# Performance work log

Hardware: AMD Instinct MI355X
Metric: run time of the kernel (lower is better)

Reference implementation:

```python
import jax, jax.numpy as jnp
import numpy as np

B, C, H, W = 64, 3, 384, 384


def setup_inputs() -> dict:
    key = jax.random.key(0)
    k1, k2 = jax.random.split(key)
    imgs = jax.random.normal(k1, (B, C, H, W), dtype=jnp.float32)
    eye = jnp.broadcast_to(jnp.eye(2, 3, dtype=jnp.float32), (B, 2, 3))
    theta = eye + 0.05 * jax.random.normal(k2, (B, 2, 3), dtype=jnp.float32)
    return {"imgs": imgs, "theta": theta}


def _gen_affine_grid(theta, h, w):
    # Mirrors torchvision functional_tensor._gen_affine_grid (align_corners=False style).
    # theta: [2,3]; returns normalized grid [h, w, 2] in [-1, 1].
    d = 0.5
    xs = jnp.linspace(-w * 0.5 + d, w * 0.5 + d - 1, w, dtype=jnp.float32)  # [w]
    ys = jnp.linspace(-h * 0.5 + d, h * 0.5 + d - 1, h, dtype=jnp.float32)  # [h]
    # base_grid[y, x] = (xs[x], ys[y], 1)
    xg, yg = jnp.meshgrid(xs, ys)  # each [h, w]
    ones = jnp.ones_like(xg)
    base = jnp.stack([xg, yg, ones], axis=-1)  # [h, w, 3]
    scale = jnp.array([0.5 * w, 0.5 * h], dtype=jnp.float32)
    rescaled_theta = theta.T / scale  # [3, 2]
    return base @ rescaled_theta  # [h, w, 2]


def _grid_sample_bilinear(img, grid):
    # img: [C, H, W], grid: [H, W, 2] normalized coords, zeros padding,
    # align_corners=False (torch grid_sample semantics).
    c, h, w = img.shape
    ix = (grid[..., 0] + 1.0) * w * 0.5 - 0.5  # [H, W]
    iy = (grid[..., 1] + 1.0) * h * 0.5 - 0.5
    x0 = jnp.floor(ix)
    y0 = jnp.floor(iy)
    wx1 = ix - x0
    wy1 = iy - y0
    wx0 = 1.0 - wx1
    wy0 = 1.0 - wy1

    def gather(xi, yi):
        valid = (xi >= 0) & (xi < w) & (yi >= 0) & (yi < h)
        xc = jnp.clip(xi, 0, w - 1).astype(jnp.int32)
        yc = jnp.clip(yi, 0, h - 1).astype(jnp.int32)
        v = img[:, yc, xc]  # [C, H, W] gather
        return v * valid.astype(img.dtype)

    out = (gather(x0, y0) * (wx0 * wy0)
           + gather(x0 + 1, y0) * (wx1 * wy0)
           + gather(x0, y0 + 1) * (wx0 * wy1)
           + gather(x0 + 1, y0 + 1) * (wx1 * wy1))
    return out  # [C, H, W]


def reference(imgs, theta):
    b, c, h, w = imgs.shape

    def per_image(img, th):
        grid = _gen_affine_grid(th, h, w)
        return _grid_sample_bilinear(img, grid)

    return jax.vmap(per_image)(imgs, theta)  # [B, C, H, W]
```

## Files before the change

kernel.cpp:

```cpp
#include <hip/hip_runtime.h>

#define B_ 64
#define C_ 3
#define H_ 384
#define W_ 384
#define HW_ (H_ * W_)

__global__ __launch_bounds__(256) void affine_sample_kernel(
    const float* __restrict__ imgs,
    const float* __restrict__ theta,
    float* __restrict__ out)
{
    int nb = gridDim.x;
    int bid = blockIdx.x;
    int sb = (bid & 7) * (nb >> 3) + (bid >> 3);

    int idx = sb * 256 + threadIdx.x;
    int x = idx % W_;
    int t = idx / W_;
    int y = t % H_;
    int b = t / H_;
    b = __builtin_amdgcn_readfirstlane(b);

    const float* th = theta + b * 6;
    float t00 = th[0], t01 = th[1], t02 = th[2];
    float t10 = th[3], t11 = th[4], t12 = th[5];

    float xg = (float)x - 191.5f;
    float yg = (float)y - 191.5f;

    float ix = fmaf(xg, t00, fmaf(yg, t01, t02)) + 191.5f;
    float iy = fmaf(xg, t10, fmaf(yg, t11, t12)) + 191.5f;

    float x0f = floorf(ix);
    float y0f = floorf(iy);
    float wx1 = ix - x0f;
    float wy1 = iy - y0f;
    float wx0 = 1.0f - wx1;
    float wy0 = 1.0f - wy1;
    float x1f = x0f + 1.0f;
    float y1f = y0f + 1.0f;

    bool vx0 = (x0f >= 0.0f) && (x0f < (float)W_);
    bool vx1 = (x1f >= 0.0f) && (x1f < (float)W_);
    bool vy0 = (y0f >= 0.0f) && (y0f < (float)H_);
    bool vy1 = (y1f >= 0.0f) && (y1f < (float)H_);

    int x0 = (int)fminf(fmaxf(x0f, 0.0f), (float)(W_ - 1));
    int x1 = (int)fminf(fmaxf(x1f, 0.0f), (float)(W_ - 1));
    int y0 = (int)fminf(fmaxf(y0f, 0.0f), (float)(H_ - 1));
    int y1 = (int)fminf(fmaxf(y1f, 0.0f), (float)(H_ - 1));

    float w00 = wx0 * wy0 * ((vx0 && vy0) ? 1.0f : 0.0f);
    float w01 = wx1 * wy0 * ((vx1 && vy0) ? 1.0f : 0.0f);
    float w10 = wx0 * wy1 * ((vx0 && vy1) ? 1.0f : 0.0f);
    float w11 = wx1 * wy1 * ((vx1 && vy1) ? 1.0f : 0.0f);

    int o00 = y0 * W_ + x0;
    int o01 = y0 * W_ + x1;
    int o10 = y1 * W_ + x0;
    int o11 = y1 * W_ + x1;

    const float* bimg = imgs + (size_t)b * (C_ * HW_);
    float* bout = out + (size_t)b * (C_ * HW_) + y * W_ + x;

    float v[C_][4];
#pragma unroll
    for (int c = 0; c < C_; ++c) {
        const float* p = bimg + c * HW_;
        v[c][0] = p[o00];
        v[c][1] = p[o01];
        v[c][2] = p[o10];
        v[c][3] = p[o11];
    }

#pragma unroll
    for (int c = 0; c < C_; ++c) {
        float r = fmaf(v[c][0], w00, fmaf(v[c][1], w01,
                  fmaf(v[c][2], w10, v[c][3] * w11)));
        bout[c * HW_] = r;
    }
}

extern "C" void kernel_launch(void* const* d_in, const int* in_sizes, int n_in,
                              void* d_out, int out_size, void* d_ws, size_t ws_size,
                              hipStream_t stream) {
    const float* imgs = (const float*)d_in[0];
    const float* theta = (const float*)d_in[1];
    float* out = (float*)d_out;
    int total = B_ * H_ * W_;
    affine_sample_kernel<<<total / 256, 256, 0, stream>>>(imgs, theta, out);
}
```

Baseline: 224.1 us.

## Process 2x2 output pixels per thread with vector nontemporal stores

Each thread now computes a 2x2 block of output pixels, so a 192-thread block covers two full rows, and the grid shrinks to one block per row pair. The four bilinear setups share the theta loads and index math, and the outputs go out as 2-wide vector nontemporal stores. The aim is fewer threads, wider stores, and more independent gathers in flight per thread. In exchange, register pressure rises and each wave's gather addresses span two rows, which may change cache locality.

Measured after the change: 253.2 us. 1.13x slower.

```diff
diff --git a/kernel.cpp b/kernel.cpp
--- a/kernel.cpp
+++ b/kernel.cpp
@@ -6,29 +6,15 @@
 #define W_ 384
 #define HW_ (H_ * W_)
 
-__global__ __launch_bounds__(256) void affine_sample_kernel(
-    const float* __restrict__ imgs,
-    const float* __restrict__ theta,
-    float* __restrict__ out)
+typedef float f32x2 __attribute__((ext_vector_type(2)));
+
+struct Pix { float w00, w01, w10, w11; int o00, o01, o10, o11; };
+
+__device__ __forceinline__ Pix pix_setup(
+    float xg, float yg,
+    float t00, float t01, float t02,
+    float t10, float t11, float t12)
 {
-    int nb = gridDim.x;
-    int bid = blockIdx.x;
-    int sb = (bid & 7) * (nb >> 3) + (bid >> 3);
-
-    int idx = sb * 256 + threadIdx.x;
-    int x = idx % W_;
-    int t = idx / W_;
-    int y = t % H_;
-    int b = t / H_;
-    b = __builtin_amdgcn_readfirstlane(b);
-
-    const float* th = theta + b * 6;
-    float t00 = th[0], t01 = th[1], t02 = th[2];
-    float t10 = th[3], t11 = th[4], t12 = th[5];
-
-    float xg = (float)x - 191.5f;
-    float yg = (float)y - 191.5f;
-
     float ix = fmaf(xg, t00, fmaf(yg, t01, t02)) + 191.5f;
     float iy = fmaf(xg, t10, fmaf(yg, t11, t12)) + 191.5f;
 
@@ -51,34 +37,66 @@
     int y0 = (int)fminf(fmaxf(y0f, 0.0f), (float)(H_ - 1));
     int y1 = (int)fminf(fmaxf(y1f, 0.0f), (float)(H_ - 1));
 
-    float w00 = wx0 * wy0 * ((vx0 && vy0) ? 1.0f : 0.0f);
-    float w01 = wx1 * wy0 * ((vx1 && vy0) ? 1.0f : 0.0f);
-    float w10 = wx0 * wy1 * ((vx0 && vy1) ? 1.0f : 0.0f);
-    float w11 = wx1 * wy1 * ((vx1 && vy1) ? 1.0f : 0.0f);
+    Pix p;
+    p.w00 = wx0 * wy0 * ((vx0 && vy0) ? 1.0f : 0.0f);
+    p.w01 = wx1 * wy0 * ((vx1 && vy0) ? 1.0f : 0.0f);
+    p.w10 = wx0 * wy1 * ((vx0 && vy1) ? 1.0f : 0.0f);
+    p.w11 = wx1 * wy1 * ((vx1 && vy1) ? 1.0f : 0.0f);
+    p.o00 = y0 * W_ + x0;
+    p.o01 = y0 * W_ + x1;
+    p.o10 = y1 * W_ + x0;
+    p.o11 = y1 * W_ + x1;
+    return p;
+}
 
-    int o00 = y0 * W_ + x0;
-    int o01 = y0 * W_ + x1;
-    int o10 = y1 * W_ + x0;
-    int o11 = y1 * W_ + x1;
+__global__ __launch_bounds__(192) void affine_sample_kernel(
+    const float* __restrict__ imgs,
+    const float* __restrict__ theta,
+    float* __restrict__ out)
+{
+    int nb = gridDim.x;
+    int bid = blockIdx.x;
+    int sb = (bid & 7) * (nb >> 3) + (bid >> 3);
+
+    int b  = sb / 192;
+    int yp = sb - b * 192;
+    b = __builtin_amdgcn_readfirstlane(b);
+    int y = yp * 2;
+    int x = threadIdx.x * 2;
+
+    const float* th = theta + b * 6;
+    float t00 = th[0], t01 = th[1], t02 = th[2];
+    float t10 = th[3], t11 = th[4], t12 = th[5];
+
+    float xg = (float)x - 191.5f;
+    float yg = (float)y - 191.5f;
+
+    Pix pa = pix_setup(xg,        yg,        t00, t01, t02, t10, t11, t12);
+    Pix pb = pix_setup(xg + 1.0f, yg,        t00, t01, t02, t10, t11, t12);
+    Pix pc = pix_setup(xg,        yg + 1.0f, t00, t01, t02, t10, t11, t12);
+    Pix pd = pix_setup(xg + 1.0f, yg + 1.0f, t00, t01, t02, t10, t11, t12);
 
     const float* bimg = imgs + (size_t)b * (C_ * HW_);
     float* bout = out + (size_t)b * (C_ * HW_) + y * W_ + x;
 
-    float v[C_][4];
 #pragma unroll
     for (int c = 0; c < C_; ++c) {
         const float* p = bimg + c * HW_;
-        v[c][0] = p[o00];
-        v[c][1] = p[o01];
-        v[c][2] = p[o10];
-        v[c][3] = p[o11];
-    }
 
-#pragma unroll
-    for (int c = 0; c < C_; ++c) {
-        float r = fmaf(v[c][0], w00, fmaf(v[c][1], w01,
-                  fmaf(v[c][2], w10, v[c][3] * w11)));
-        bout[c * HW_] = r;
+        float a0 = p[pa.o00], a1 = p[pa.o01], a2 = p[pa.o10], a3 = p[pa.o11];
+        float b0 = p[pb.o00], b1 = p[pb.o01], b2 = p[pb.o10], b3 = p[pb.o11];
+        float c0 = p[pc.o00], c1 = p[pc.o01], c2 = p[pc.o10], c3 = p[pc.o11];
+        float d0 = p[pd.o00], d1 = p[pd.o01], d2 = p[pd.o10], d3 = p[pd.o11];
+
+        float ra = fmaf(a0, pa.w00, fmaf(a1, pa.w01, fmaf(a2, pa.w10, a3 * pa.w11)));
+        float rb = fmaf(b0, pb.w00, fmaf(b1, pb.w01, fmaf(b2, pb.w10, b3 * pb.w11)));
+        float rc = fmaf(c0, pc.w00, fmaf(c1, pc.w01, fmaf(c2, pc.w10, c3 * pc.w11)));
+        float rd = fmaf(d0, pd.w00, fmaf(d1, pd.w01, fmaf(d2, pd.w10, d3 * pd.w11)));
+
+        f32x2 top; top.x = ra; top.y = rb;
+        f32x2 bot; bot.x = rc; bot.y = rd;
+        __builtin_nontemporal_store(top, reinterpret_cast<f32x2*>(bout + c * HW_));
+        __builtin_nontemporal_store(bot, reinterpret_cast<f32x2*>(bout + c * HW_ + W_));
     }
 }
 
@@ -88,6 +106,6 @@
     const float* imgs = (const float*)d_in[0];
     const float* theta = (const float*)d_in[1];
     float* out = (float*)d_out;
-    int total = B_ * H_ * W_;
-    affine_sample_kernel<<<total / 256, 256, 0, stream>>>(imgs, theta, out);
+    int blocks = B_ * (H_ / 2);
+    affine_sample_kernel<<<blocks, 192, 0, stream>>>(imgs, theta, out);
 }
```

## Compute two adjacent pixels per thread with shared 4-wide row loads

Applied to the files above, without the earlier changes.

Each thread now produces two horizontally adjacent output pixels, tiled as 128x4 blocks. It fetches 4-wide unaligned vector loads of the two source rows, plus an optional third row, and picks the bilinear taps with selects instead of issuing four scalar gathers per pixel. A fallback path does per-pixel 2-wide loads when the taps do not fit the shared window. Output is written with 8-byte vector stores. The aim is fewer memory instructions and better coalescing, at the cost of extra ALU select work, more registers, and a divergent fallback.

Result: faster. 208.4 us (-7.0%).

```diff
diff --git a/kernel.cpp b/kernel.cpp
--- a/kernel.cpp
+++ b/kernel.cpp
@@ -6,32 +6,24 @@
 #define W_ 384
 #define HW_ (H_ * W_)
 
-__global__ __launch_bounds__(256) void affine_sample_kernel(
-    const float* __restrict__ imgs,
-    const float* __restrict__ theta,
-    float* __restrict__ out)
+typedef float f32x4 __attribute__((ext_vector_type(4)));
+typedef float f32x2 __attribute__((ext_vector_type(2)));
+typedef f32x4 __attribute__((aligned(4))) f32x4_u;
+typedef f32x2 __attribute__((aligned(4))) f32x2_u;
+typedef f32x2 __attribute__((aligned(8))) f32x2_a8;
+
+__device__ __forceinline__ float sel3(int d, float a, float b, float c) {
+    return d == 0 ? a : (d == 1 ? b : c);
+}
+
+struct PixS {
+    float w00, w01, w10, w11;
+    int   xb, y0, y1;
+    bool  selx0, selx1;
+};
+
+__device__ __forceinline__ PixS pix_setup(float ix, float iy)
 {
-    int nb = gridDim.x;
-    int bid = blockIdx.x;
-    int sb = (bid & 7) * (nb >> 3) + (bid >> 3);
-
-    int idx = sb * 256 + threadIdx.x;
-    int x = idx % W_;
-    int t = idx / W_;
-    int y = t % H_;
-    int b = t / H_;
-    b = __builtin_amdgcn_readfirstlane(b);
-
-    const float* th = theta + b * 6;
-    float t00 = th[0], t01 = th[1], t02 = th[2];
-    float t10 = th[3], t11 = th[4], t12 = th[5];
-
-    float xg = (float)x - 191.5f;
-    float yg = (float)y - 191.5f;
-
-    float ix = fmaf(xg, t00, fmaf(yg, t01, t02)) + 191.5f;
-    float iy = fmaf(xg, t10, fmaf(yg, t11, t12)) + 191.5f;
-
     float x0f = floorf(ix);
     float y0f = floorf(iy);
     float wx1 = ix - x0f;
@@ -48,37 +40,143 @@
 
     int x0 = (int)fminf(fmaxf(x0f, 0.0f), (float)(W_ - 1));
     int x1 = (int)fminf(fmaxf(x1f, 0.0f), (float)(W_ - 1));
-    int y0 = (int)fminf(fmaxf(y0f, 0.0f), (float)(H_ - 1));
-    int y1 = (int)fminf(fmaxf(y1f, 0.0f), (float)(H_ - 1));
+    PixS p;
+    p.y0 = (int)fminf(fmaxf(y0f, 0.0f), (float)(H_ - 1));
+    p.y1 = (int)fminf(fmaxf(y1f, 0.0f), (float)(H_ - 1));
+    p.xb = (int)fminf(fmaxf(x0f, 0.0f), (float)(W_ - 2));
+    p.selx0 = (x0 == p.xb);
+    p.selx1 = (x1 == p.xb);
+    p.w00 = wx0 * wy0 * ((vx0 && vy0) ? 1.0f : 0.0f);
+    p.w01 = wx1 * wy0 * ((vx1 && vy0) ? 1.0f : 0.0f);
+    p.w10 = wx0 * wy1 * ((vx0 && vy1) ? 1.0f : 0.0f);
+    p.w11 = wx1 * wy1 * ((vx1 && vy1) ? 1.0f : 0.0f);
+    return p;
+}
 
-    float w00 = wx0 * wy0 * ((vx0 && vy0) ? 1.0f : 0.0f);
-    float w01 = wx1 * wy0 * ((vx1 && vy0) ? 1.0f : 0.0f);
-    float w10 = wx0 * wy1 * ((vx0 && vy1) ? 1.0f : 0.0f);
-    float w11 = wx1 * wy1 * ((vx1 && vy1) ? 1.0f : 0.0f);
+__global__ __launch_bounds__(256) void affine_sample_kernel(
+    const float* __restrict__ imgs,
+    const float* __restrict__ theta,
+    float* __restrict__ out)
+{
+    int nb = gridDim.x;
+    int bid = blockIdx.x;
+    int sb = (bid & 7) * (nb >> 3) + (bid >> 3);
 
-    int o00 = y0 * W_ + x0;
-    int o01 = y0 * W_ + x1;
-    int o10 = y1 * W_ + x0;
-    int o11 = y1 * W_ + x1;
+    int b   = sb / 288;
+    int rem = sb - b * 288;
+    int yt  = rem / 3;
+    int xt  = rem - yt * 3;
+    b = __builtin_amdgcn_readfirstlane(b);
+
+    int tid = threadIdx.x;
+    int x = xt * 128 + ((tid & 63) << 1);
+    int y = yt * 4 + (tid >> 6);
+
+    const float* th = theta + b * 6;
+    float t00 = th[0], t01 = th[1], t02 = th[2];
+    float t10 = th[3], t11 = th[4], t12 = th[5];
+
+    float xg0 = (float)x - 191.5f;
+    float xg1 = xg0 + 1.0f;
+    float yg  = (float)y - 191.5f;
+
+    float ix0 = fmaf(xg0, t00, fmaf(yg, t01, t02)) + 191.5f;
+    float iy0 = fmaf(xg0, t10, fmaf(yg, t11, t12)) + 191.5f;
+    float ix1 = fmaf(xg1, t00, fmaf(yg, t01, t02)) + 191.5f;
+    float iy1 = fmaf(xg1, t10, fmaf(yg, t11, t12)) + 191.5f;
+
+    PixS p0 = pix_setup(ix0, iy0);
+    PixS p1 = pix_setup(ix1, iy1);
+
+    int xq = p0.xb < p1.xb ? p0.xb : p1.xb;
+    if (xq > W_ - 4) xq = W_ - 4;
+    int d0 = p0.xb - xq;
+    int d1 = p1.xb - xq;
+
+    bool needT = (p1.y0 != p0.y0) && (p1.y0 != p0.y1);
+    bool needB = (p1.y1 != p0.y1) && (p1.y1 != p0.y0);
+    int  rX    = needT ? p1.y0 : p1.y1;
+    bool needX = needT || needB;
+    bool ok = (d0 <= 2) && (d1 <= 2) && !(needT && needB && (p1.y1 != p1.y0));
 
     const float* bimg = imgs + (size_t)b * (C_ * HW_);
-    float* bout = out + (size_t)b * (C_ * HW_) + y * W_ + x;
+    int aoff = p0.y0 * W_ + xq;
+    int boff = p0.y1 * W_ + xq;
+    int xoff = rX    * W_ + xq;
 
-    float v[C_][4];
+    f32x4 Av[3], Bv[3], Xv[3];
 #pragma unroll
     for (int c = 0; c < C_; ++c) {
-        const float* p = bimg + c * HW_;
-        v[c][0] = p[o00];
-        v[c][1] = p[o01];
-        v[c][2] = p[o10];
-        v[c][3] = p[o11];
+        Av[c] = *reinterpret_cast<const f32x4_u*>(bimg + c * HW_ + aoff);
+        Bv[c] = *reinterpret_cast<const f32x4_u*>(bimg + c * HW_ + boff);
+        Xv[c] = Av[c];
+    }
+    if (needX) {
+#pragma unroll
+        for (int c = 0; c < C_; ++c)
+            Xv[c] = *reinterpret_cast<const f32x4_u*>(bimg + c * HW_ + xoff);
     }
 
+    bool selT_A = (p1.y0 == p0.y0);
+    bool selT_B = (p1.y0 == p0.y1);
+    bool selB_B = (p1.y1 == p0.y1);
+    bool selB_A = (p1.y1 == p0.y0);
+
+    float r[2][3];
 #pragma unroll
     for (int c = 0; c < C_; ++c) {
-        float r = fmaf(v[c][0], w00, fmaf(v[c][1], w01,
-                  fmaf(v[c][2], w10, v[c][3] * w11)));
-        bout[c * HW_] = r;
+        f32x4 A = Av[c], Bq = Bv[c], X = Xv[c];
+        float t0a = sel3(d0, A.x, A.y, A.z),  t0b = sel3(d0, A.y, A.z, A.w);
+        float b0a = sel3(d0, Bq.x, Bq.y, Bq.z), b0b = sel3(d0, Bq.y, Bq.z, Bq.w);
+        float v00 = p0.selx0 ? t0a : t0b;
+        float v01 = p0.selx1 ? t0a : t0b;
+        float v10 = p0.selx0 ? b0a : b0b;
+        float v11 = p0.selx1 ? b0a : b0b;
+        r[0][c] = fmaf(v00, p0.w00, fmaf(v01, p0.w01,
+                  fmaf(v10, p0.w10, v11 * p0.w11)));
+        float eAa = sel3(d1, A.x, A.y, A.z),  eAb = sel3(d1, A.y, A.z, A.w);
+        float eBa = sel3(d1, Bq.x, Bq.y, Bq.z), eBb = sel3(d1, Bq.y, Bq.z, Bq.w);
+        float eXa = sel3(d1, X.x, X.y, X.z),  eXb = sel3(d1, X.y, X.z, X.w);
+        float t1a = selT_A ? eAa : (selT_B ? eBa : eXa);
+        float t1b = selT_A ? eAb : (selT_B ? eBb : eXb);
+        float b1a = selB_B ? eBa : (selB_A ? eAa : eXa);
+        float b1b = selB_B ? eBb : (selB_A ? eAb : eXb);
+        float u00 = p1.selx0 ? t1a : t1b;
+        float u01 = p1.selx1 ? t1a : t1b;
+        float u10 = p1.selx0 ? b1a : b1b;
+        float u11 = p1.selx1 ? b1a : b1b;
+        r[1][c] = fmaf(u00, p1.w00, fmaf(u01, p1.w01,
+                  fmaf(u10, p1.w10, u11 * p1.w11)));
+    }
+
+    if (__builtin_expect(!ok, 0)) {
+#pragma unroll
+        for (int c = 0; c < C_; ++c) {
+            const float* pch = bimg + c * HW_;
+            f32x2 vt = *reinterpret_cast<const f32x2_u*>(pch + p0.y0 * W_ + p0.xb);
+            f32x2 vb = *reinterpret_cast<const f32x2_u*>(pch + p0.y1 * W_ + p0.xb);
+            float v00 = p0.selx0 ? vt.x : vt.y;
+            float v01 = p0.selx1 ? vt.x : vt.y;
+            float v10 = p0.selx0 ? vb.x : vb.y;
+            float v11 = p0.selx1 ? vb.x : vb.y;
+            r[0][c] = fmaf(v00, p0.w00, fmaf(v01, p0.w01,
+                      fmaf(v10, p0.w10, v11 * p0.w11)));
+            f32x2 ut = *reinterpret_cast<const f32x2_u*>(pch + p1.y0 * W_ + p1.xb);
+            f32x2 ub = *reinterpret_cast<const f32x2_u*>(pch + p1.y1 * W_ + p1.xb);
+            float u00 = p1.selx0 ? ut.x : ut.y;
+            float u01 = p1.selx1 ? ut.x : ut.y;
+            float u10 = p1.selx0 ? ub.x : ub.y;
+            float u11 = p1.selx1 ? ub.x : ub.y;
+            r[1][c] = fmaf(u00, p1.w00, fmaf(u01, p1.w01,
+                      fmaf(u10, p1.w10, u11 * p1.w11)));
+        }
+    }
+
+    float* bout = out + (size_t)b * (C_ * HW_) + (size_t)y * W_ + x;
+#pragma unroll
+    for (int c = 0; c < C_; ++c) {
+        f32x2 o; o.x = r[0][c]; o.y = r[1][c];
+        *reinterpret_cast<f32x2_a8*>(bout + c * HW_) = o;
     }
 }
 
@@ -88,6 +186,6 @@
     const float* imgs = (const float*)d_in[0];
     const float* theta = (const float*)d_in[1];
     float* out = (float*)d_out;
-    int total = B_ * H_ * W_;
-    affine_sample_kernel<<<total / 256, 256, 0, stream>>>(imgs, theta, out);
+    int blocks = B_ * 96 * 3;
+    affine_sample_kernel<<<blocks, 256, 0, stream>>>(imgs, theta, out);
 }
```
